# Kernel optimization log

Measured on AMD Instinct MI355X. Metric: run time of the kernel, lower is better.

## Reference

```python
import jax, jax.numpy as jnp
import numpy as np
import math

H = 16        # num heads
D = 64        # head dim
HID = 1024    # hidden size
MULT = 2      # GIN MLP multiplier
FRAC = 0.1    # top_k fraction of available predecessors
THR = 0.2     # threshold value
BASE = 10000.0  # rope base
CHUNK = 32    # query-row chunk for max aggregator
NEG = -1e30


def _rope(x, pos):
    # x: (b, H, S, D); pos: (b, S) int
    d = x.shape[-1]
    inv = 1.0 / (BASE ** (jnp.arange(0, d, 2, dtype=jnp.float32) / d))
    ang = pos.astype(jnp.float32)[..., None] * inv            # (b, S, d//2)
    cos = jnp.concatenate([jnp.cos(ang)] * 2, -1)[:, None]    # (b, 1, S, d)
    sin = jnp.concatenate([jnp.sin(ang)] * 2, -1)[:, None]
    x1, x2 = jnp.split(x, 2, axis=-1)
    return x * cos + jnp.concatenate([-x2, x1], -1) * sin


def _scaled_topk_causal(adj):
    # faithful vectorization of scaled_topk_causal_4d: per query row i, keep
    # top max(1, ceil(FRAC*i)) of the (threshold-filtered) strict predecessors.
    S = adj.shape[-1]
    j = jnp.arange(S)
    strict = j[None, :] < j[:, None]                           # (S, S) j < i
    # torch: filtered = a[:, :i] * (a >= thr)  -> below-threshold become 0
    filtered = jnp.where(strict, jnp.where(adj >= THR, adj, 0.0), NEG)
    order = jnp.argsort(-filtered, axis=-1)                    # descending, stable
    rank = jnp.argsort(order, axis=-1)                         # inverse permutation
    k = jnp.maximum(1, jnp.ceil(FRAC * jnp.arange(S, dtype=jnp.float32))).astype(jnp.int32)
    k = k.at[0].set(0)                                         # row 0 has no predecessors
    return ((rank < k[None, None, :, None]) & strict).astype(adj.dtype)


def reference(hidden_states, Wq, Wk, Wv, Wo, W1, W2, eps, position_ids):
    b, S, _ = hidden_states.shape
    q = (hidden_states @ Wq).reshape(b, S, H, D).transpose(0, 2, 1, 3)
    kk = (hidden_states @ Wk).reshape(b, S, H, D).transpose(0, 2, 1, 3)
    v = (hidden_states @ Wv).reshape(b, S, H, D).transpose(0, 2, 1, 3)
    q = _rope(q, position_ids)
    kk = _rope(kk, position_ids)
    scores = jnp.einsum('bhid,bhjd->bhij', q, kk) / math.sqrt(D)
    adj = _scaled_topk_causal(scores)                          # binary (b,H,S,S)
    deg = adj.sum(-1)                                          # (b,H,S)
    denom = jnp.maximum(deg, 1.0)[..., None]
    s_agg = jnp.einsum('bhij,bhjd->bhid', adj, v)              # sum
    m_agg = s_agg / denom                                      # mean
    var = jnp.maximum(jnp.einsum('bhij,bhjd->bhid', adj, v * v) / denom - m_agg ** 2, 0.0)
    # max aggregator: masked max over selected predecessors, chunked over rows
    nc = S // CHUNK
    adj_c = jnp.moveaxis(adj.reshape(b, H, nc, CHUNK, S), 2, 0)  # (nc,b,H,C,S)
    mx = jax.lax.map(
        lambda ac: jnp.max(jnp.where(ac[..., None] > 0, v[:, :, None, :, :], NEG), axis=-2),
        adj_c)                                                 # (nc,b,H,C,D)
    mx = jnp.moveaxis(mx, 0, 2).reshape(b, H, S, D)
    mx = jnp.where(deg[..., None] > 0, mx, 0.0)
    comb = jnp.concatenate([s_agg, m_agg, mx, var], -1)        # (b,H,S,4D)
    h1 = jax.nn.silu(jnp.einsum('bhsf,hfm->bhsm', comb, W1))   # per-head GIN MLP
    head_out = jnp.einsum('bhsm,hmd->bhsd', h1, W2) + eps * v  # epsilon-scaled residual
    return head_out.transpose(0, 2, 1, 3).reshape(b, S, H * D) @ Wo


def setup_inputs() -> dict:
    key = jax.random.key(0)
    ks = jax.random.split(key, 8)
    b, S = 1, 1024
    sc = 0.02
    return {
        'hidden_states': jax.random.normal(ks[0], (b, S, HID), jnp.float32),
        'Wq': jax.random.normal(ks[1], (HID, H * D), jnp.float32) * sc,
        'Wk': jax.random.normal(ks[2], (HID, H * D), jnp.float32) * sc,
        'Wv': jax.random.normal(ks[3], (HID, H * D), jnp.float32) * sc,
        'Wo': jax.random.normal(ks[4], (H * D, HID), jnp.float32) * sc,
        'W1': jax.random.normal(ks[5], (H, 4 * D, MULT * D), jnp.float32) * sc,
        'W2': jax.random.normal(ks[6], (H, MULT * D, D), jnp.float32) * sc,
        'eps': jnp.asarray(0.1, jnp.float32),
        'position_ids': jnp.arange(S, dtype=jnp.int32)[None, :],
    }
```

## Files before the change

kernel.cpp:

```cpp
#include <hip/hip_runtime.h>
#include <math.h>

#define NEGF  -1e30f
#define TAU   1e-6f

static __device__ __forceinline__ int imin(int a, int b) { return a < b ? a : b; }

static __device__ __forceinline__ void fma44(float A[4][4], const float4 xa, const float4 yb) {
  A[0][0] += xa.x * yb.x; A[0][1] += xa.x * yb.y; A[0][2] += xa.x * yb.z; A[0][3] += xa.x * yb.w;
  A[1][0] += xa.y * yb.x; A[1][1] += xa.y * yb.y; A[1][2] += xa.y * yb.z; A[1][3] += xa.y * yb.w;
  A[2][0] += xa.z * yb.x; A[2][1] += xa.z * yb.y; A[2][2] += xa.z * yb.z; A[2][3] += xa.z * yb.w;
  A[3][0] += xa.w * yb.x; A[3][1] += xa.w * yb.y; A[3][2] += xa.w * yb.z; A[3][3] += xa.w * yb.w;
}

static __device__ __forceinline__ void fold44(float T[4][4], float A[4][4]) {
#pragma unroll
  for (int e = 0; e < 4; ++e)
#pragma unroll
    for (int f = 0; f < 4; ++f) { T[e][f] = __fadd_rn(T[e][f], A[e][f]); A[e][f] = 0.0f; }
}

template <int MODE>
__global__ __launch_bounds__(256) void gemm64(
    const float* __restrict__ A, const float* __restrict__ B, float* __restrict__ C,
    const float* __restrict__ R, const float* __restrict__ eps_p,
    int M, int N, int K, int lda, int ldb, int ldc,
    long sA, long sB, long sC)
{
  const int z = blockIdx.z;
  A += (long)z * sA;
  B += (long)z * sB;
  float* Cf = C + (long)z * sC;
  const float* Rz = (MODE == 2) ? (R + (long)z * sC) : nullptr;

  const int bm = blockIdx.x * 64;
  const int bn = blockIdx.y * 64;
  const int tid = threadIdx.x;
  const int r0 = (tid >> 4) * 4;
  const int c0 = (tid & 15) * 4;

  __shared__ float As[16][68];
  __shared__ float Bs[16][64];

  float acc[4][4] = {};

  const int ar = tid >> 2;
  const int ac = (tid & 3) * 4;
  const int br = tid >> 4;
  const int bc = (tid & 15) * 4;

  for (int kt = 0; kt < K; kt += 16) {
    float4 av = *(const float4*)(A + (long)(bm + ar) * lda + kt + ac);
    float4 bv = *(const float4*)(B + (long)(kt + br) * ldb + bn + bc);
    As[ac + 0][ar] = av.x;
    As[ac + 1][ar] = av.y;
    As[ac + 2][ar] = av.z;
    As[ac + 3][ar] = av.w;
    *(float4*)&Bs[br][bc] = bv;
    __syncthreads();
#pragma unroll
    for (int kk = 0; kk < 16; ++kk) {
      const float4 xa = *(const float4*)&As[kk][r0];
      const float4 yb = *(const float4*)&Bs[kk][c0];
      fma44(acc, xa, yb);
    }
    __syncthreads();
  }

  const float ev = (MODE == 2) ? eps_p[0] : 0.0f;
#pragma unroll
  for (int e = 0; e < 4; ++e)
#pragma unroll
    for (int f = 0; f < 4; ++f) {
      const int r = bm + r0 + e;
      const int c = bn + c0 + f;
      float x = acc[e][f];
      if (MODE == 1) x = x / (1.0f + expf(-x));
      if (MODE == 2) x += ev * Rz[(long)r * ldc + c];
      Cf[(long)r * ldc + c] = x;
    }
}

__global__ __launch_bounds__(256) void gemm_qkv64(
    const float* __restrict__ A,
    const float* __restrict__ Wq, const float* __restrict__ Wk, const float* __restrict__ Wv,
    float* __restrict__ qo, float* __restrict__ ko, float* __restrict__ vo)
{
  const int z = blockIdx.z;
  const float* B = (z == 0) ? Wq : (z == 1) ? Wk : Wv;
  float* C = (z == 0) ? qo : (z == 1) ? ko : vo;

  const int bm = blockIdx.x * 64;
  const int bn = blockIdx.y * 64;
  const int tid = threadIdx.x;
  const int r0 = (tid >> 4) * 4;
  const int c0 = (tid & 15) * 4;

  __shared__ float As[2][32][68];
  __shared__ float Bs[2][32][64];

  float acc[4][4] = {};
  float tot[4][4] = {};

  const int ar = tid >> 2;
  const int ac = (tid & 3) * 8;
  const int br = tid >> 3;
  const int bc = (tid & 7) * 8;

  {
    float4 a0 = *(const float4*)(A + (long)(bm + ar) * 1024 + ac);
    float4 a1 = *(const float4*)(A + (long)(bm + ar) * 1024 + ac + 4);
    float4 b0 = *(const float4*)(B + (long)br * 1024 + bn + bc);
    float4 b1 = *(const float4*)(B + (long)br * 1024 + bn + bc + 4);
    As[0][ac + 0][ar] = a0.x; As[0][ac + 1][ar] = a0.y;
    As[0][ac + 2][ar] = a0.z; As[0][ac + 3][ar] = a0.w;
    As[0][ac + 4][ar] = a1.x; As[0][ac + 5][ar] = a1.y;
    As[0][ac + 6][ar] = a1.z; As[0][ac + 7][ar] = a1.w;
    *(float4*)&Bs[0][br][bc] = b0;
    *(float4*)&Bs[0][br][bc + 4] = b1;
  }
  __syncthreads();

  int cur = 0;
  for (int kt = 0; kt < 1024; kt += 32) {
    const bool more = (kt + 32 < 1024);
    float4 a0n, a1n, b0n, b1n;
    if (more) {
      a0n = *(const float4*)(A + (long)(bm + ar) * 1024 + kt + 32 + ac);
      a1n = *(const float4*)(A + (long)(bm + ar) * 1024 + kt + 32 + ac + 4);
      b0n = *(const float4*)(B + (long)(kt + 32 + br) * 1024 + bn + bc);
      b1n = *(const float4*)(B + (long)(kt + 32 + br) * 1024 + bn + bc + 4);
    }
    if (kt == 384 || kt == 768) {
      fold44(tot, acc);
    }
#pragma unroll
    for (int kk = 0; kk < 32; ++kk) {
      const float4 xa = *(const float4*)&As[cur][kk][r0];
      const float4 yb = *(const float4*)&Bs[cur][kk][c0];
      fma44(acc, xa, yb);
    }
    if (more) {
      const int nxt = cur ^ 1;
      As[nxt][ac + 0][ar] = a0n.x; As[nxt][ac + 1][ar] = a0n.y;
      As[nxt][ac + 2][ar] = a0n.z; As[nxt][ac + 3][ar] = a0n.w;
      As[nxt][ac + 4][ar] = a1n.x; As[nxt][ac + 5][ar] = a1n.y;
      As[nxt][ac + 6][ar] = a1n.z; As[nxt][ac + 7][ar] = a1n.w;
      *(float4*)&Bs[nxt][br][bc] = b0n;
      *(float4*)&Bs[nxt][br][bc + 4] = b1n;
      __syncthreads();
      cur = nxt;
    }
  }

#pragma unroll
  for (int e = 0; e < 4; ++e)
#pragma unroll
    for (int f = 0; f < 4; ++f)
      C[(long)(bm + r0 + e) * 1024 + bn + c0 + f] = __fadd_rn(tot[e][f], acc[e][f]);
}

__global__ __launch_bounds__(256) void combine_out(
    const float4* __restrict__ p, float4* __restrict__ dst)
{
  const int idx = blockIdx.x * 256 + threadIdx.x;
  const float4 a = p[idx];
  const float4 b = p[idx + (1 << 18)];
  float4 r;
  r.x = __fadd_rn(a.x, b.x);
  r.y = __fadd_rn(a.y, b.y);
  r.z = __fadd_rn(a.z, b.z);
  r.w = __fadd_rn(a.w, b.w);
  dst[idx] = r;
}

__global__ __launch_bounds__(256) void rope_table(
    const int* __restrict__ pos_ids, float2* __restrict__ tab)
{
  const int g = blockIdx.x * 256 + threadIdx.x;
  const int t = g & 31;
  const int s = g >> 5;

  const float e = (float)(2 * t) / 64.0f;
  const float p32 = (float)pow(10000.0, (double)e);
  const float inv = __fdiv_rn(1.0f, p32);
  const float posf = (float)pos_ids[s];
  const float ang = __fmul_rn(posf, inv);
  tab[g] = make_float2((float)cos((double)ang), (float)sin((double)ang));
}

__global__ __launch_bounds__(256) void rope_apply(float* __restrict__ q,
                                                  float* __restrict__ kb,
                                                  const float2* __restrict__ tab)
{
  const int g = blockIdx.x * blockDim.x + threadIdx.x;
  const int t = g & 31;
  const int h = (g >> 5) & 15;
  const int s = (g >> 9) & 1023;
  const int buf = g >> 19;
  float* p = buf ? kb : q;

  const float2 cs = tab[s * 32 + t];
  const float c  = cs.x;
  const float sn = cs.y;

  const int base = s * 1024 + h * 64;
  const float x1 = p[base + t];
  const float x2 = p[base + t + 32];
  p[base + t]      = __fadd_rn(__fmul_rn(x1, c), __fmul_rn(-x2, sn));
  p[base + t + 32] = __fadd_rn(__fmul_rn(x2, c), __fmul_rn(x1, sn));
}

__global__ __launch_bounds__(256) void gemm_score(
    const float* __restrict__ q, const float* __restrict__ kb,
    float* __restrict__ S, int headBase)
{
  const int x = blockIdx.x;
  int bmT = 0;
  while ((bmT + 1) * (bmT + 2) / 2 <= x) ++bmT;
  const int bnT = x - bmT * (bmT + 1) / 2;

  const int hl = blockIdx.y;
  const int off = (headBase + hl) * 64;
  const int bm = bmT * 64;
  const int bn = bnT * 64;
  const int tid = threadIdx.x;
  const int r0 = (tid >> 4) * 4;
  const int c0 = (tid & 15) * 4;

  __shared__ float As[16][68];
  __shared__ float Bs[16][68];

  float acc[4][4] = {};

  const int ar = tid >> 2;
  const int ac = (tid & 3) * 4;

  for (int kt = 0; kt < 64; kt += 16) {
    float4 av = *(const float4*)(q  + (long)(bm + ar) * 1024 + off + kt + ac);
    float4 bv = *(const float4*)(kb + (long)(bn + ar) * 1024 + off + kt + ac);
    As[ac + 0][ar] = av.x; As[ac + 1][ar] = av.y;
    As[ac + 2][ar] = av.z; As[ac + 3][ar] = av.w;
    Bs[ac + 0][ar] = bv.x; Bs[ac + 1][ar] = bv.y;
    Bs[ac + 2][ar] = bv.z; Bs[ac + 3][ar] = bv.w;
    __syncthreads();
#pragma unroll
    for (int kk = 0; kk < 16; ++kk) {
      const float4 xa = *(const float4*)&As[kk][r0];
      const float4 yb = *(const float4*)&Bs[kk][c0];
      fma44(acc, xa, yb);
    }
    __syncthreads();
  }

#pragma unroll
  for (int e = 0; e < 4; ++e)
#pragma unroll
    for (int f = 0; f < 4; ++f)
      S[((long)hl * 1024 + bm + r0 + e) * 1024 + bn + c0 + f] = acc[e][f] * 0.125f;
}

__global__ __launch_bounds__(256) void select_agg2(
    const float* __restrict__ S, const float* __restrict__ v,
    float* __restrict__ comb, int headBase)
{
  const int i = blockIdx.x;
  const int hl = blockIdx.y;
  const int h = headBase + hl;
  const int tid = threadIdx.x;
  const int lane = tid & 63;
  const int wid = tid >> 6;

  __shared__ int hist[256];
  __shared__ int wtot[4];
  __shared__ int selBinSh, newRkSh, selCntSh;
  __shared__ unsigned vminSh;
  __shared__ int mInIdx;
  __shared__ unsigned WBits;
  __shared__ int outIdxMin;
  __shared__ unsigned long long tbIn, tbOut;
  __shared__ int hypOut, hypIn;
  __shared__ int listLen;
  __shared__ unsigned list[128];
  __shared__ float red[6][4][64];

  if (tid == 0) {
    mInIdx = -1; WBits = 0u; outIdxMin = 0x7FFFFFFF;
    tbIn = ~0ull; tbOut = ~0ull; hypOut = -1; hypIn = -1; listLen = 0;
  }

  const int cs = (i + 255) >> 8;
  const int j0 = tid * cs;
  const int j1 = imin(j0 + cs, i);
  const int nj = (j1 > j0) ? (j1 - j0) : 0;

  float rawr[4];
  unsigned uf[4];
  const float* row = S + ((long)hl * 1024 + i) * 1024;
#pragma unroll
  for (int m = 0; m < 4; ++m) {
    const float rv = (m < nj) ? row[j0 + m] : 0.0f;
    rawr[m] = rv;
    uf[m] = (m < nj) ? __float_as_uint((rv >= 0.2f) ? rv : 0.0f) : 0u;
  }

  const int kk = (i > 0) ? (i + 9) / 10 : 0;
  unsigned V = 0u;
  int need_eq = 0;
  int f0[4] = {0, 0, 0, 0};

  if (kk > 0) {
    unsigned prefix = 0;
    int rk = kk;
    bool done = false;
    for (int pass = 0; pass < 4 && !done; ++pass) {
      const int shift = 24 - 8 * pass;
      hist[tid] = 0;
      __syncthreads();
      if (pass == 0) {
        int zc = 0;
#pragma unroll
        for (int m = 0; m < 4; ++m) if (m < nj) {
          const unsigned u = uf[m];
          if (u) atomicAdd(&hist[u >> 24], 1); else ++zc;
        }
#pragma unroll
        for (int off = 32; off >= 1; off >>= 1) zc += __shfl_xor(zc, off, 64);
        if (lane == 0 && zc) atomicAdd(&hist[0], zc);
      } else {
#pragma unroll
        for (int m = 0; m < 4; ++m) if (m < nj) {
          const unsigned u = uf[m];
          if (u != 0u && (u >> (shift + 8)) == prefix) atomicAdd(&hist[(u >> shift) & 0xFF], 1);
        }
      }
      __syncthreads();
      const int hval = hist[tid];
      int val = hval;
#pragma unroll
      for (int off = 1; off < 64; off <<= 1) {
        int n = __shfl_up(val, off, 64);
        if (lane >= off) val += n;
      }
      if (lane == 63) wtot[wid] = val;
      __syncthreads();
      int wpre = 0;
      for (int w = 0; w < wid; ++w) wpre += wtot[w];
      const int incl = wpre + val;
      const int total = wtot[0] + wtot[1] + wtot[2] + wtot[3];
      const int sfx = total - incl + hval;
      if (sfx >= rk && (sfx - hval) < rk) {
        selBinSh = tid;
        newRkSh = rk - (sfx - hval);
        selCntSh = hval;
      }
      __syncthreads();
      const int selBin = selBinSh;
      prefix = (prefix << 8) | (unsigned)selBin;
      rk = newRkSh;
      const int scnt = selCntSh;
      if (pass == 0 && selBin == 0) {
        V = 0u; need_eq = rk; done = true;
      } else if (rk == scnt) {
        if (tid == 0) vminSh = 0xFFFFFFFFu;
        __syncthreads();
#pragma unroll
        for (int m = 0; m < 4; ++m) if (m < nj) {
          const unsigned u = uf[m];
          if (u != 0u && (u >> shift) == prefix) atomicMin(&vminSh, u);
        }
        __syncthreads();
        V = vminSh; need_eq = 0x3FFFFFFF; done = true;
      }
    }
    if (!done) { V = prefix; need_eq = rk; }

    int e = 0;
#pragma unroll
    for (int m = 0; m < 4; ++m) if (m < nj) { if (uf[m] == V) ++e; }
    int val = e;
#pragma unroll
    for (int off = 1; off < 64; off <<= 1) {
      int n = __shfl_up(val, off, 64);
      if (lane >= off) val += n;
    }
    if (lane == 63) wtot[wid] = val;
    __syncthreads();
    int wpre = 0;
    for (int w = 0; w < wid; ++w) wpre += wtot[w];
    int excl = wpre + val - e;
#pragma unroll
    for (int m = 0; m < 4; ++m) if (m < nj) {
      const unsigned u = uf[m];
      if (u > V) f0[m] = 1;
      else if (u == V) { if (excl < need_eq) f0[m] = 1; ++excl; }
    }
  }
  __syncthreads();

  if (kk > 0 && kk < i) {
    unsigned wmax = 0u;
#pragma unroll
    for (int m = 0; m < 4; ++m) if (m < nj) {
      const int j = j0 + m;
      const unsigned u = uf[m];
      if (f0[m]) {
        if (u == V) atomicMax(&mInIdx, j);
        const float fv = __uint_as_float(u);
        const float dd = fv - 0.2f;
        if (fv >= 0.2f && dd < TAU)
          atomicMin(&tbIn, (((unsigned long long)__float_as_uint(dd)) << 32) | (unsigned)j);
      } else {
        wmax = (u > wmax) ? u : wmax;
        if (rawr[m] < 0.2f) {
          const float dd = 0.2f - rawr[m];
          if (dd < TAU)
            atomicMin(&tbOut, (((unsigned long long)__float_as_uint(dd)) << 32) | (unsigned)j);
        }
      }
    }
#pragma unroll
    for (int off = 32; off >= 1; off >>= 1) {
      unsigned o = (unsigned)__shfl_xor((int)wmax, off, 64);
      wmax = (o > wmax) ? o : wmax;
    }
    if (lane == 0) atomicMax(&WBits, wmax);
    __syncthreads();
#pragma unroll
    for (int m = 0; m < 4; ++m) if (m < nj) {
      const int j = j0 + m;
      if (!f0[m] && uf[m] == WBits) atomicMin(&outIdxMin, j);
    }
    __syncthreads();
    if (tid == 0) {
      float bestD = TAU;
      int oI = -1, nI = -1;
      if (outIdxMin != 0x7FFFFFFF && mInIdx >= 0) {
        const float Vf = __uint_as_float(V);
        const float Wf = __uint_as_float(WBits);
        if (!(WBits == V && V == 0u)) {
          const float gapA = Vf - Wf;
          if (gapA < bestD) { bestD = gapA; oI = mInIdx; nI = outIdxMin; }
        }
        if (tbIn != ~0ull) {
          const float d = __uint_as_float((unsigned)(tbIn >> 32));
          const int jj = (int)(tbIn & 0xFFFFFFFFu);
          const bool noop = (WBits == 0u && jj < outIdxMin);
          if (!noop && d < bestD) { bestD = d; oI = jj; nI = outIdxMin; }
        }
        if (tbOut != ~0ull && Vf <= 0.2f) {
          const float d = __uint_as_float((unsigned)(tbOut >> 32));
          const int jj = (int)(tbOut & 0xFFFFFFFFu);
          if (d < bestD) { bestD = d; oI = mInIdx; nI = jj; }
        }
      }
      hypOut = oI; hypIn = nI;
    }
  }
  __syncthreads();

  const bool amb = (hypOut >= 0);
  int cnt = 0;
#pragma unroll
  for (int m = 0; m < 4; ++m) if (m < nj) {
    const int j = j0 + m;
    int s1 = f0[m];
    if (amb) { if (j == hypOut) s1 = 0; if (j == hypIn) s1 = 1; }
    if (f0[m] | s1) ++cnt;
  }
  {
    int val = cnt;
#pragma unroll
    for (int off = 1; off < 64; off <<= 1) {
      int n = __shfl_up(val, off, 64);
      if (lane >= off) val += n;
    }
    if (lane == 63) wtot[wid] = val;
    __syncthreads();
    int wpre = 0;
    for (int w = 0; w < wid; ++w) wpre += wtot[w];
    int base = wpre + val - cnt;
#pragma unroll
    for (int m = 0; m < 4; ++m) if (m < nj) {
      const int j = j0 + m;
      int s1 = f0[m];
      if (amb) { if (j == hypOut) s1 = 0; if (j == hypIn) s1 = 1; }
      if (f0[m] | s1) {
        list[base] = (unsigned)j | ((unsigned)f0[m] << 10) | ((unsigned)s1 << 11);
        ++base;
      }
    }
    if (tid == 0) listLen = wtot[0] + wtot[1] + wtot[2] + wtot[3];
  }
  __syncthreads();

  const int L = listLen;
  float sum0 = 0, sq0 = 0, mx0 = NEGF, sum1 = 0, sq1 = 0, mx1 = NEGF;
  for (int e2 = wid; e2 < L; e2 += 4) {
    const unsigned en = list[e2];
    const int j = en & 1023;
    const float vv = v[(long)j * 1024 + h * 64 + lane];
    if (en & (1u << 10)) { sum0 += vv; sq0 += vv * vv; mx0 = fmaxf(mx0, vv); }
    if (en & (1u << 11)) { sum1 += vv; sq1 += vv * vv; mx1 = fmaxf(mx1, vv); }
  }
  red[0][wid][lane] = sum0; red[1][wid][lane] = sq0; red[2][wid][lane] = mx0;
  red[3][wid][lane] = sum1; red[4][wid][lane] = sq1; red[5][wid][lane] = mx1;
  __syncthreads();

  if (tid < 64) {
    float S0 = 0, Q0 = 0, M0 = NEGF, S1 = 0, Q1 = 0, M1 = NEGF;
#pragma unroll
    for (int gg = 0; gg < 4; ++gg) {
      S0 += red[0][gg][tid]; Q0 += red[1][gg][tid]; M0 = fmaxf(M0, red[2][gg][tid]);
      S1 += red[3][gg][tid]; Q1 += red[4][gg][tid]; M1 = fmaxf(M1, red[5][gg][tid]);
    }
    const float denom = (float)(kk > 0 ? kk : 1);
    const float mean0 = S0 / denom, mean1 = S1 / denom;
    const float var0 = fmaxf(Q0 / denom - mean0 * mean0, 0.0f);
    const float var1 = fmaxf(Q1 / denom - mean1 * mean1, 0.0f);
    const float mx0o = (kk > 0) ? M0 : 0.0f;
    const float mx1o = (kk > 0) ? M1 : 0.0f;
    float* crow = comb + ((long)(h * 1024 + i)) * 256;
    crow[tid]       = 0.5f * (S0 + S1);
    crow[64 + tid]  = 0.5f * (mean0 + mean1);
    crow[128 + tid] = 0.5f * (mx0o + mx1o);
    crow[192 + tid] = 0.5f * (var0 + var1);
  }
}

extern "C" void kernel_launch(void* const* d_in, const int* in_sizes, int n_in,
                              void* d_out, int out_size, void* d_ws, size_t ws_size,
                              hipStream_t stream)
{
  const float* hidden = (const float*)d_in[0];
  const float* Wq = (const float*)d_in[1];
  const float* Wk = (const float*)d_in[2];
  const float* Wv = (const float*)d_in[3];
  const float* Wo = (const float*)d_in[4];
  const float* W1 = (const float*)d_in[5];
  const float* W2 = (const float*)d_in[6];
  const float* eps = (const float*)d_in[7];
  const int* pos = (const int*)d_in[8];

  const size_t MB = 1024UL * 1024UL;
  int G = 4;
  if (ws_size >= 28 * MB + 64 * MB) G = 16;
  else if (ws_size >= 28 * MB + 32 * MB) G = 8;

  float* q      = (float*)d_ws;
  float* kbuf   = q + (1 << 20);
  float* v      = kbuf + (1 << 20);
  float* comb   = v + (1 << 20);
  float* scores = comb + (1 << 22);
  float* h1     = scores;
  float* ho     = scores + (1 << 21);
  float2* tab   = (float2*)comb;
  float* parts  = comb;

  const dim3 blk(256);

  gemm_qkv64<<<dim3(16, 16, 3), blk, 0, stream>>>(hidden, Wq, Wk, Wv, q, kbuf, v);

  rope_table<<<128, blk, 0, stream>>>(pos, tab);
  rope_apply<<<4096, blk, 0, stream>>>(q, kbuf, tab);

  for (int g = 0; g < 16; g += G) {
    gemm_score<<<dim3(136, G), blk, 0, stream>>>(q, kbuf, scores, g);
    select_agg2<<<dim3(1024, G), blk, 0, stream>>>(scores, v, comb, g);
  }

  gemm64<1><<<dim3(16, 2, 16), blk, 0, stream>>>(comb, W1, h1, nullptr, nullptr,
      1024, 128, 256, 256, 128, 128, (long)1024 * 256, (long)256 * 128, (long)1024 * 128);

  gemm64<2><<<dim3(16, 1, 16), blk, 0, stream>>>(h1, W2, ho, v, eps,
      1024, 64, 128, 128, 64, 1024, (long)1024 * 128, (long)128 * 64, 64);

  gemm64<0><<<dim3(16, 16, 2), blk, 0, stream>>>(ho, Wo, parts, nullptr, nullptr,
      1024, 1024, 512, 1024, 1024, 1024, 512, (long)512 * 1024, (long)1 << 20);
  combine_out<<<dim3(1024), blk, 0, stream>>>((const float4*)parts, (float4*)d_out);
}
```

Measured before the change: 382.5 us.

## Process one query row per wavefront in top-k selection kernel

The selection/aggregation kernel now assigns each query row to a single 64-lane wavefront, four rows per block, instead of one row per 256-thread block. This removes all block-level __syncthreads and shared-memory reductions in favour of wave shuffles and per-wave histograms, and loads each row with vectorized float4 reads. The value gather is unrolled four entries at a time. In exchange each lane holds 16 elements in registers, which raises register pressure, and the gather for a row is now serialized within one wave.

```diff
diff --git a/kernel.cpp b/kernel.cpp
--- a/kernel.cpp
+++ b/kernel.cpp
@@ -260,54 +260,50 @@
       S[((long)hl * 1024 + bm + r0 + e) * 1024 + bn + c0 + f] = acc[e][f] * 0.125f;
 }
 
-__global__ __launch_bounds__(256) void select_agg2(
+__global__ __launch_bounds__(256) void select_agg3(
     const float* __restrict__ S, const float* __restrict__ v,
     float* __restrict__ comb, int headBase)
 {
-  const int i = blockIdx.x;
-  const int hl = blockIdx.y;
-  const int h = headBase + hl;
   const int tid = threadIdx.x;
   const int lane = tid & 63;
   const int wid = tid >> 6;
-
-  __shared__ int hist[256];
-  __shared__ int wtot[4];
-  __shared__ int selBinSh, newRkSh, selCntSh;
-  __shared__ unsigned vminSh;
-  __shared__ int mInIdx;
-  __shared__ unsigned WBits;
-  __shared__ int outIdxMin;
-  __shared__ unsigned long long tbIn, tbOut;
-  __shared__ int hypOut, hypIn;
-  __shared__ int listLen;
-  __shared__ unsigned list[128];
-  __shared__ float red[6][4][64];
-
-  if (tid == 0) {
-    mInIdx = -1; WBits = 0u; outIdxMin = 0x7FFFFFFF;
-    tbIn = ~0ull; tbOut = ~0ull; hypOut = -1; hypIn = -1; listLen = 0;
-  }
-
-  const int cs = (i + 255) >> 8;
-  const int j0 = tid * cs;
-  const int j1 = imin(j0 + cs, i);
-  const int nj = (j1 > j0) ? (j1 - j0) : 0;
-
-  float rawr[4];
-  unsigned uf[4];
+  const int i = blockIdx.x * 4 + wid;
+  const int hl = blockIdx.y;
+  const int h = headBase + hl;
+
+  __shared__ int histS[4][256];
+  __shared__ unsigned listS[4][128];
+  int* hist = histS[wid];
+  unsigned* list = listS[wid];
+
+  const int jb = lane * 16;
+  const int njc = i - jb;
+  const int nj = njc < 0 ? 0 : (njc > 16 ? 16 : njc);
+
   const float* row = S + ((long)hl * 1024 + i) * 1024;
-#pragma unroll
-  for (int m = 0; m < 4; ++m) {
-    const float rv = (m < nj) ? row[j0 + m] : 0.0f;
-    rawr[m] = rv;
-    uf[m] = (m < nj) ? __float_as_uint((rv >= 0.2f) ? rv : 0.0f) : 0u;
+  float raw[16];
+  unsigned uf[16];
+  {
+    const float4 r0 = *(const float4*)(row + jb);
+    const float4 r1 = *(const float4*)(row + jb + 4);
+    const float4 r2 = *(const float4*)(row + jb + 8);
+    const float4 r3 = *(const float4*)(row + jb + 12);
+    raw[0]=r0.x; raw[1]=r0.y; raw[2]=r0.z; raw[3]=r0.w;
+    raw[4]=r1.x; raw[5]=r1.y; raw[6]=r1.z; raw[7]=r1.w;
+    raw[8]=r2.x; raw[9]=r2.y; raw[10]=r2.z; raw[11]=r2.w;
+    raw[12]=r3.x; raw[13]=r3.y; raw[14]=r3.z; raw[15]=r3.w;
+  }
+#pragma unroll
+  for (int m = 0; m < 16; ++m) {
+    const float rv = (m < nj) ? raw[m] : 0.0f;
+    raw[m] = rv;
+    uf[m] = (m < nj && rv >= 0.2f) ? __float_as_uint(rv) : 0u;
   }
 
   const int kk = (i > 0) ? (i + 9) / 10 : 0;
   unsigned V = 0u;
   int need_eq = 0;
-  int f0[4] = {0, 0, 0, 0};
+  unsigned fmask = 0u;
 
   if (kk > 0) {
     unsigned prefix = 0;
@@ -315,217 +311,223 @@
     bool done = false;
     for (int pass = 0; pass < 4 && !done; ++pass) {
       const int shift = 24 - 8 * pass;
-      hist[tid] = 0;
-      __syncthreads();
-      if (pass == 0) {
-        int zc = 0;
-#pragma unroll
-        for (int m = 0; m < 4; ++m) if (m < nj) {
-          const unsigned u = uf[m];
-          if (u) atomicAdd(&hist[u >> 24], 1); else ++zc;
+      *(int4*)&hist[lane * 4] = make_int4(0, 0, 0, 0);
+      asm volatile("s_waitcnt lgkmcnt(0)" ::: "memory");
+      __builtin_amdgcn_sched_barrier(0);
+#pragma unroll
+      for (int m = 0; m < 16; ++m) {
+        const unsigned u = uf[m];
+        if (m < nj && u != 0u && (pass == 0 || (u >> (shift + 8)) == prefix))
+          atomicAdd(&hist[(u >> shift) & 0xFF], 1);
+      }
+      asm volatile("s_waitcnt lgkmcnt(0)" ::: "memory");
+      __builtin_amdgcn_sched_barrier(0);
+      const int4 hv = *(const int4*)&hist[lane * 4];
+      const int s = hv.x + hv.y + hv.z + hv.w;
+      int suf = s;
+#pragma unroll
+      for (int off = 1; off < 64; off <<= 1) {
+        const int o = __shfl_down(suf, off, 64);
+        if (lane + off < 64) suf += o;
+      }
+      const int tot = __shfl(suf, 0, 64);
+      if (pass == 0 && tot < rk) {
+        V = 0u; need_eq = rk - tot; done = true;
+      } else {
+        const int above = suf - s;
+        const int sfx3 = above + hv.w;
+        const int sfx2 = sfx3 + hv.z;
+        const int sfx1 = sfx2 + hv.y;
+        const int sfx0 = suf;
+        int mbin = -1, mh = 0, msfx = 0;
+        if (!(pass == 0 && lane == 0) && sfx0 >= rk && sfx0 - hv.x < rk) { mbin = lane * 4 + 0; mh = hv.x; msfx = sfx0; }
+        if (sfx1 >= rk && sfx1 - hv.y < rk) { mbin = lane * 4 + 1; mh = hv.y; msfx = sfx1; }
+        if (sfx2 >= rk && sfx2 - hv.z < rk) { mbin = lane * 4 + 2; mh = hv.z; msfx = sfx2; }
+        if (sfx3 >= rk && sfx3 - hv.w < rk) { mbin = lane * 4 + 3; mh = hv.w; msfx = sfx3; }
+        const unsigned long long bal = __ballot(mbin >= 0);
+        const int src = (int)__ffsll((unsigned long long)bal) - 1;
+        const int selBin = __shfl(mbin, src, 64) & 0xFF;
+        const int scnt = __shfl(mh, src, 64);
+        const int ssfx = __shfl(msfx, src, 64);
+        prefix = (prefix << 8) | (unsigned)selBin;
+        rk = rk - (ssfx - scnt);
+        if (rk == scnt) {
+          unsigned vm = 0xFFFFFFFFu;
+#pragma unroll
+          for (int m = 0; m < 16; ++m) {
+            const unsigned u = uf[m];
+            if (m < nj && u != 0u && (u >> shift) == prefix && u < vm) vm = u;
+          }
+#pragma unroll
+          for (int off = 1; off < 64; off <<= 1) {
+            const unsigned o = (unsigned)__shfl_xor((int)vm, off, 64);
+            if (o < vm) vm = o;
+          }
+          V = vm; need_eq = 0x3FFFFFFF; done = true;
         }
-#pragma unroll
-        for (int off = 32; off >= 1; off >>= 1) zc += __shfl_xor(zc, off, 64);
-        if (lane == 0 && zc) atomicAdd(&hist[0], zc);
-      } else {
-#pragma unroll
-        for (int m = 0; m < 4; ++m) if (m < nj) {
-          const unsigned u = uf[m];
-          if (u != 0u && (u >> (shift + 8)) == prefix) atomicAdd(&hist[(u >> shift) & 0xFF], 1);
-        }
-      }
-      __syncthreads();
-      const int hval = hist[tid];
-      int val = hval;
-#pragma unroll
-      for (int off = 1; off < 64; off <<= 1) {
-        int n = __shfl_up(val, off, 64);
-        if (lane >= off) val += n;
-      }
-      if (lane == 63) wtot[wid] = val;
-      __syncthreads();
-      int wpre = 0;
-      for (int w = 0; w < wid; ++w) wpre += wtot[w];
-      const int incl = wpre + val;
-      const int total = wtot[0] + wtot[1] + wtot[2] + wtot[3];
-      const int sfx = total - incl + hval;
-      if (sfx >= rk && (sfx - hval) < rk) {
-        selBinSh = tid;
-        newRkSh = rk - (sfx - hval);
-        selCntSh = hval;
-      }
-      __syncthreads();
-      const int selBin = selBinSh;
-      prefix = (prefix << 8) | (unsigned)selBin;
-      rk = newRkSh;
-      const int scnt = selCntSh;
-      if (pass == 0 && selBin == 0) {
-        V = 0u; need_eq = rk; done = true;
-      } else if (rk == scnt) {
-        if (tid == 0) vminSh = 0xFFFFFFFFu;
-        __syncthreads();
-#pragma unroll
-        for (int m = 0; m < 4; ++m) if (m < nj) {
-          const unsigned u = uf[m];
-          if (u != 0u && (u >> shift) == prefix) atomicMin(&vminSh, u);
-        }
-        __syncthreads();
-        V = vminSh; need_eq = 0x3FFFFFFF; done = true;
       }
     }
     if (!done) { V = prefix; need_eq = rk; }
 
     int e = 0;
 #pragma unroll
-    for (int m = 0; m < 4; ++m) if (m < nj) { if (uf[m] == V) ++e; }
+    for (int m = 0; m < 16; ++m) if (m < nj && uf[m] == V) ++e;
     int val = e;
 #pragma unroll
     for (int off = 1; off < 64; off <<= 1) {
-      int n = __shfl_up(val, off, 64);
+      const int n = __shfl_up(val, off, 64);
       if (lane >= off) val += n;
     }
-    if (lane == 63) wtot[wid] = val;
-    __syncthreads();
-    int wpre = 0;
-    for (int w = 0; w < wid; ++w) wpre += wtot[w];
-    int excl = wpre + val - e;
-#pragma unroll
-    for (int m = 0; m < 4; ++m) if (m < nj) {
+    int excl = val - e;
+#pragma unroll
+    for (int m = 0; m < 16; ++m) if (m < nj) {
       const unsigned u = uf[m];
-      if (u > V) f0[m] = 1;
-      else if (u == V) { if (excl < need_eq) f0[m] = 1; ++excl; }
-    }
-  }
-  __syncthreads();
-
+      if (u > V) fmask |= (1u << m);
+      else if (u == V) { if (excl < need_eq) fmask |= (1u << m); ++excl; }
+    }
+  }
+
+  int hypOut = -1, hypIn = -1;
   if (kk > 0 && kk < i) {
     unsigned wmax = 0u;
-#pragma unroll
-    for (int m = 0; m < 4; ++m) if (m < nj) {
-      const int j = j0 + m;
+    int mIn = -1;
+    unsigned long long tbIn = ~0ull, tbOut = ~0ull;
+#pragma unroll
+    for (int m = 0; m < 16; ++m) if (m < nj) {
+      const int j = jb + m;
       const unsigned u = uf[m];
-      if (f0[m]) {
-        if (u == V) atomicMax(&mInIdx, j);
+      if ((fmask >> m) & 1u) {
+        if (u == V && j > mIn) mIn = j;
         const float fv = __uint_as_float(u);
         const float dd = fv - 0.2f;
-        if (fv >= 0.2f && dd < TAU)
-          atomicMin(&tbIn, (((unsigned long long)__float_as_uint(dd)) << 32) | (unsigned)j);
+        if (fv >= 0.2f && dd < TAU) {
+          const unsigned long long p = (((unsigned long long)__float_as_uint(dd)) << 32) | (unsigned)j;
+          if (p < tbIn) tbIn = p;
+        }
       } else {
-        wmax = (u > wmax) ? u : wmax;
-        if (rawr[m] < 0.2f) {
-          const float dd = 0.2f - rawr[m];
-          if (dd < TAU)
-            atomicMin(&tbOut, (((unsigned long long)__float_as_uint(dd)) << 32) | (unsigned)j);
+        if (u > wmax) wmax = u;
+        if (raw[m] < 0.2f) {
+          const float dd = 0.2f - raw[m];
+          if (dd < TAU) {
+            const unsigned long long p = (((unsigned long long)__float_as_uint(dd)) << 32) | (unsigned)j;
+            if (p < tbOut) tbOut = p;
+          }
         }
       }
     }
 #pragma unroll
-    for (int off = 32; off >= 1; off >>= 1) {
-      unsigned o = (unsigned)__shfl_xor((int)wmax, off, 64);
-      wmax = (o > wmax) ? o : wmax;
-    }
-    if (lane == 0) atomicMax(&WBits, wmax);
-    __syncthreads();
-#pragma unroll
-    for (int m = 0; m < 4; ++m) if (m < nj) {
-      const int j = j0 + m;
-      if (!f0[m] && uf[m] == WBits) atomicMin(&outIdxMin, j);
-    }
-    __syncthreads();
-    if (tid == 0) {
-      float bestD = TAU;
-      int oI = -1, nI = -1;
-      if (outIdxMin != 0x7FFFFFFF && mInIdx >= 0) {
-        const float Vf = __uint_as_float(V);
-        const float Wf = __uint_as_float(WBits);
-        if (!(WBits == V && V == 0u)) {
-          const float gapA = Vf - Wf;
-          if (gapA < bestD) { bestD = gapA; oI = mInIdx; nI = outIdxMin; }
-        }
-        if (tbIn != ~0ull) {
-          const float d = __uint_as_float((unsigned)(tbIn >> 32));
-          const int jj = (int)(tbIn & 0xFFFFFFFFu);
-          const bool noop = (WBits == 0u && jj < outIdxMin);
-          if (!noop && d < bestD) { bestD = d; oI = jj; nI = outIdxMin; }
-        }
-        if (tbOut != ~0ull && Vf <= 0.2f) {
-          const float d = __uint_as_float((unsigned)(tbOut >> 32));
-          const int jj = (int)(tbOut & 0xFFFFFFFFu);
-          if (d < bestD) { bestD = d; oI = mInIdx; nI = jj; }
-        }
-      }
-      hypOut = oI; hypIn = nI;
-    }
-  }
-  __syncthreads();
+    for (int off = 1; off < 64; off <<= 1) {
+      const unsigned ow = (unsigned)__shfl_xor((int)wmax, off, 64);
+      if (ow > wmax) wmax = ow;
+      const int om = __shfl_xor(mIn, off, 64);
+      if (om > mIn) mIn = om;
+      const unsigned long long oi = __shfl_xor(tbIn, off, 64);
+      if (oi < tbIn) tbIn = oi;
+      const unsigned long long oo = __shfl_xor(tbOut, off, 64);
+      if (oo < tbOut) tbOut = oo;
+    }
+    int outMin = 0x7FFFFFFF;
+#pragma unroll
+    for (int m = 0; m < 16; ++m) if (m < nj) {
+      if (!((fmask >> m) & 1u) && uf[m] == wmax) {
+        const int j = jb + m;
+        if (j < outMin) outMin = j;
+      }
+    }
+#pragma unroll
+    for (int off = 1; off < 64; off <<= 1) {
+      const int o = __shfl_xor(outMin, off, 64);
+      if (o < outMin) outMin = o;
+    }
+    float bestD = TAU;
+    int oI = -1, nI = -1;
+    if (outMin != 0x7FFFFFFF && mIn >= 0) {
+      const float Vf = __uint_as_float(V);
+      const float Wf = __uint_as_float(wmax);
+      if (!(wmax == V && V == 0u)) {
+        const float gapA = Vf - Wf;
+        if (gapA < bestD) { bestD = gapA; oI = mIn; nI = outMin; }
+      }
+      if (tbIn != ~0ull) {
+        const float d = __uint_as_float((unsigned)(tbIn >> 32));
+        const int jj = (int)(tbIn & 0xFFFFFFFFu);
+        const bool noop = (wmax == 0u && jj < outMin);
+        if (!noop && d < bestD) { bestD = d; oI = jj; nI = outMin; }
+      }
+      if (tbOut != ~0ull && Vf <= 0.2f) {
+        const float d = __uint_as_float((unsigned)(tbOut >> 32));
+        const int jj = (int)(tbOut & 0xFFFFFFFFu);
+        if (d < bestD) { bestD = d; oI = mIn; nI = jj; }
+      }
+    }
+    hypOut = oI; hypIn = nI;
+  }
 
   const bool amb = (hypOut >= 0);
+  unsigned smask = 0u;
   int cnt = 0;
 #pragma unroll
-  for (int m = 0; m < 4; ++m) if (m < nj) {
-    const int j = j0 + m;
-    int s1 = f0[m];
+  for (int m = 0; m < 16; ++m) if (m < nj) {
+    const int j = jb + m;
+    int s1 = (int)((fmask >> m) & 1u);
     if (amb) { if (j == hypOut) s1 = 0; if (j == hypIn) s1 = 1; }
-    if (f0[m] | s1) ++cnt;
-  }
-  {
-    int val = cnt;
-#pragma unroll
-    for (int off = 1; off < 64; off <<= 1) {
-      int n = __shfl_up(val, off, 64);
-      if (lane >= off) val += n;
-    }
-    if (lane == 63) wtot[wid] = val;
-    __syncthreads();
-    int wpre = 0;
-    for (int w = 0; w < wid; ++w) wpre += wtot[w];
-    int base = wpre + val - cnt;
-#pragma unroll
-    for (int m = 0; m < 4; ++m) if (m < nj) {
-      const int j = j0 + m;
-      int s1 = f0[m];
-      if (amb) { if (j == hypOut) s1 = 0; if (j == hypIn) s1 = 1; }
-      if (f0[m] | s1) {
-        list[base] = (unsigned)j | ((unsigned)f0[m] << 10) | ((unsigned)s1 << 11);
-        ++base;
-      }
-    }
-    if (tid == 0) listLen = wtot[0] + wtot[1] + wtot[2] + wtot[3];
-  }
-  __syncthreads();
-
-  const int L = listLen;
+    if (s1) smask |= (1u << m);
+    if (((fmask >> m) & 1u) | (unsigned)s1) ++cnt;
+  }
+  int val2 = cnt;
+#pragma unroll
+  for (int off = 1; off < 64; off <<= 1) {
+    const int n = __shfl_up(val2, off, 64);
+    if (lane >= off) val2 += n;
+  }
+  const int L = __shfl(val2, 63, 64);
+  int base = val2 - cnt;
+#pragma unroll
+  for (int m = 0; m < 16; ++m) if (m < nj) {
+    const unsigned f0b = (fmask >> m) & 1u;
+    const unsigned s1b = (smask >> m) & 1u;
+    if (f0b | s1b) {
+      list[base] = (unsigned)(jb + m) | (f0b << 10) | (s1b << 11);
+      ++base;
+    }
+  }
+  asm volatile("s_waitcnt lgkmcnt(0)" ::: "memory");
+  __builtin_amdgcn_sched_barrier(0);
+
   float sum0 = 0, sq0 = 0, mx0 = NEGF, sum1 = 0, sq1 = 0, mx1 = NEGF;
-  for (int e2 = wid; e2 < L; e2 += 4) {
-    const unsigned en = list[e2];
-    const int j = en & 1023;
-    const float vv = v[(long)j * 1024 + h * 64 + lane];
-    if (en & (1u << 10)) { sum0 += vv; sq0 += vv * vv; mx0 = fmaxf(mx0, vv); }
-    if (en & (1u << 11)) { sum1 += vv; sq1 += vv * vv; mx1 = fmaxf(mx1, vv); }
-  }
-  red[0][wid][lane] = sum0; red[1][wid][lane] = sq0; red[2][wid][lane] = mx0;
-  red[3][wid][lane] = sum1; red[4][wid][lane] = sq1; red[5][wid][lane] = mx1;
-  __syncthreads();
-
-  if (tid < 64) {
-    float S0 = 0, Q0 = 0, M0 = NEGF, S1 = 0, Q1 = 0, M1 = NEGF;
-#pragma unroll
-    for (int gg = 0; gg < 4; ++gg) {
-      S0 += red[0][gg][tid]; Q0 += red[1][gg][tid]; M0 = fmaxf(M0, red[2][gg][tid]);
-      S1 += red[3][gg][tid]; Q1 += red[4][gg][tid]; M1 = fmaxf(M1, red[5][gg][tid]);
-    }
-    const float denom = (float)(kk > 0 ? kk : 1);
-    const float mean0 = S0 / denom, mean1 = S1 / denom;
-    const float var0 = fmaxf(Q0 / denom - mean0 * mean0, 0.0f);
-    const float var1 = fmaxf(Q1 / denom - mean1 * mean1, 0.0f);
-    const float mx0o = (kk > 0) ? M0 : 0.0f;
-    const float mx1o = (kk > 0) ? M1 : 0.0f;
-    float* crow = comb + ((long)(h * 1024 + i)) * 256;
-    crow[tid]       = 0.5f * (S0 + S1);
-    crow[64 + tid]  = 0.5f * (mean0 + mean1);
-    crow[128 + tid] = 0.5f * (mx0o + mx1o);
-    crow[192 + tid] = 0.5f * (var0 + var1);
-  }
+  const float* vcol = v + h * 64 + lane;
+  for (int e2 = 0; e2 < L; e2 += 4) {
+    const uint4 en4 = *(const uint4*)&list[e2];
+    const unsigned w0 = (e2 + 0 < L) ? en4.x : 0u;
+    const unsigned w1 = (e2 + 1 < L) ? en4.y : 0u;
+    const unsigned w2 = (e2 + 2 < L) ? en4.z : 0u;
+    const unsigned w3 = (e2 + 3 < L) ? en4.w : 0u;
+    float v0 = 0, v1 = 0, v2 = 0, v3 = 0;
+    if (w0) v0 = vcol[(long)(w0 & 1023) * 1024];
+    if (w1) v1 = vcol[(long)(w1 & 1023) * 1024];
+    if (w2) v2 = vcol[(long)(w2 & 1023) * 1024];
+    if (w3) v3 = vcol[(long)(w3 & 1023) * 1024];
+    if (w0 & (1u << 10)) { sum0 += v0; sq0 += v0 * v0; mx0 = fmaxf(mx0, v0); }
+    if (w0 & (1u << 11)) { sum1 += v0; sq1 += v0 * v0; mx1 = fmaxf(mx1, v0); }
+    if (w1 & (1u << 10)) { sum0 += v1; sq0 += v1 * v1; mx0 = fmaxf(mx0, v1); }
+    if (w1 & (1u << 11)) { sum1 += v1; sq1 += v1 * v1; mx1 = fmaxf(mx1, v1); }
+    if (w2 & (1u << 10)) { sum0 += v2; sq0 += v2 * v2; mx0 = fmaxf(mx0, v2); }
+    if (w2 & (1u << 11)) { sum1 += v2; sq1 += v2 * v2; mx1 = fmaxf(mx1, v2); }
+    if (w3 & (1u << 10)) { sum0 += v3; sq0 += v3 * v3; mx0 = fmaxf(mx0, v3); }
+    if (w3 & (1u << 11)) { sum1 += v3; sq1 += v3 * v3; mx1 = fmaxf(mx1, v3); }
+  }
+
+  const float denom = (float)(kk > 0 ? kk : 1);
+  const float mean0 = sum0 / denom, mean1 = sum1 / denom;
+  const float var0 = fmaxf(sq0 / denom - mean0 * mean0, 0.0f);
+  const float var1 = fmaxf(sq1 / denom - mean1 * mean1, 0.0f);
+  const float mx0o = (kk > 0) ? mx0 : 0.0f;
+  const float mx1o = (kk > 0) ? mx1 : 0.0f;
+  float* crow = comb + ((long)(h * 1024 + i)) * 256;
+  crow[lane]       = 0.5f * (sum0 + sum1);
+  crow[64 + lane]  = 0.5f * (mean0 + mean1);
+  crow[128 + lane] = 0.5f * (mx0o + mx1o);
+  crow[192 + lane] = 0.5f * (var0 + var1);
 }
 
 extern "C" void kernel_launch(void* const* d_in, const int* in_sizes, int n_in,
@@ -566,7 +568,7 @@
 
   for (int g = 0; g < 16; g += G) {
     gemm_score<<<dim3(136, G), blk, 0, stream>>>(q, kbuf, scores, g);
-    select_agg2<<<dim3(1024, G), blk, 0, stream>>>(scores, v, comb, g);
+    select_agg3<<<dim3(256, G), blk, 0, stream>>>(scores, v, comb, g);
   }
 
   gemm64<1><<<dim3(16, 2, 16), blk, 0, stream>>>(comb, W1, h1, nullptr, nullptr,
```

Result: no change. 377.9 us (-1.2%).
